# Kernel optimization log

Measured on AMD Instinct MI355X. Metric: run time of the kernel, lower is better.

Reference implementation:

```python
import jax, jax.numpy as jnp
import numpy as np

DIM = 2048
NH = 16
HD = DIM // NH          # 128
ROPE = 64               # qk_rope_head_dim
B = 2
S = 2048
LAYER_ID = 12
LAMBDA_INIT = float(0.8 - 0.6 * np.exp(-0.3 * LAYER_ID))
EPS = 1e-5


def _rope(x, cos, sin):
    # interleaved RoPE: pairs (x[2i], x[2i+1]) rotated by angle; x: [b,s,h,ROPE]
    xr = x[..., 0::2]
    xi = x[..., 1::2]
    c = cos[None, :, None, :]  # [1,s,1,ROPE/2]
    s_ = sin[None, :, None, :]
    yr = xr * c - xi * s_
    yi = xr * s_ + xi * c
    return jnp.stack([yr, yi], axis=-1).reshape(x.shape)


def _rope_head(t, cos, sin):
    # apply RoPE to first ROPE dims of head_dim, pass-through the rest
    return jnp.concatenate([_rope(t[..., :ROPE], cos, sin), t[..., ROPE:]], axis=-1)


def setup_inputs() -> dict:
    key = jax.random.key(0)
    ks = jax.random.split(key, 10)
    inner = 2 * NH * HD
    x = jax.random.normal(ks[0], (B, S, DIM), jnp.float32)
    w_q = jax.random.normal(ks[1], (inner, DIM), jnp.float32) * (DIM ** -0.5)
    w_k = jax.random.normal(ks[2], (inner, DIM), jnp.float32) * (DIM ** -0.5)
    w_v = jax.random.normal(ks[3], (inner, DIM), jnp.float32) * (DIM ** -0.5)
    w_o = jax.random.normal(ks[4], (DIM, inner), jnp.float32) * (inner ** -0.5)
    # lambda reparameterization params (paper uses small-std init for stability)
    lambda_q1 = jax.random.normal(ks[5], (NH, HD), jnp.float32) * 0.1
    lambda_k1 = jax.random.normal(ks[6], (NH, HD), jnp.float32) * 0.1
    lambda_q2 = jax.random.normal(ks[7], (NH, HD), jnp.float32) * 0.1
    lambda_k2 = jax.random.normal(ks[8], (NH, HD), jnp.float32) * 0.1
    rms_scale = jnp.ones((NH, 2 * HD), jnp.float32)
    # rotary frequencies
    pos = jnp.arange(S, dtype=jnp.float32)
    inv_freq = 1.0 / (10000.0 ** (jnp.arange(0, ROPE, 2, dtype=jnp.float32) / ROPE))
    ang = pos[:, None] * inv_freq[None, :]  # [S, ROPE/2]
    freqs_cos = jnp.cos(ang)
    freqs_sin = jnp.sin(ang)
    # additive causal mask
    mask = jnp.triu(jnp.full((S, S), -1e9, jnp.float32), k=1)
    return dict(x=x, w_q=w_q, w_k=w_k, w_v=w_v, w_o=w_o,
                lambda_q1=lambda_q1, lambda_k1=lambda_k1,
                lambda_q2=lambda_q2, lambda_k2=lambda_k2,
                rms_scale=rms_scale, freqs_cos=freqs_cos, freqs_sin=freqs_sin,
                mask=mask)


def reference(x, w_q, w_k, w_v, w_o, lambda_q1, lambda_k1, lambda_q2, lambda_k2,
              rms_scale, freqs_cos, freqs_sin, mask):
    b, s, _ = x.shape
    q = (x @ w_q.T).reshape(b, s, NH, 2 * HD)
    k = (x @ w_k.T).reshape(b, s, NH, 2 * HD)
    v = (x @ w_v.T).reshape(b, s, NH, 2 * HD)
    q1, q2 = jnp.split(q, 2, axis=-1)
    k1, k2 = jnp.split(k, 2, axis=-1)
    q1 = _rope_head(q1, freqs_cos, freqs_sin)
    q2 = _rope_head(q2, freqs_cos, freqs_sin)
    k1 = _rope_head(k1, freqs_cos, freqs_sin)
    k2 = _rope_head(k2, freqs_cos, freqs_sin)
    # start_pos = 0 prefill -> cache slice equals current k/v
    scale = HD ** -0.5
    s1 = jnp.einsum('bqhd,bkhd->bhqk', q1, k1) * scale + mask[None, None]
    s2 = jnp.einsum('bqhd,bkhd->bhqk', q2, k2) * scale + mask[None, None]
    a1 = jax.nn.softmax(s1, axis=-1)
    a2 = jax.nn.softmax(s2, axis=-1)
    lam1 = jnp.exp(jnp.sum(lambda_q1 * lambda_k1, axis=-1))  # [NH]
    lam2 = jnp.exp(jnp.sum(lambda_q2 * lambda_k2, axis=-1))
    lam = lam1 - lam2 + LAMBDA_INIT
    attn = a1 - lam[None, :, None, None] * a2
    o = jnp.einsum('bhqk,bkhd->bqhd', attn, v)  # [b,s,NH,2*HD]
    # headwise RMSNorm over 2*head_dim, then (1 - lambda_init) scaling
    o = o * jax.lax.rsqrt(jnp.mean(o * o, axis=-1, keepdims=True) + EPS)
    o = o * rms_scale[None, None] * (1.0 - LAMBDA_INIT)
    return o.reshape(b, s, 2 * NH * HD) @ w_o.T
```

## Files before the change

### kernel.cpp

```cpp
#include <hip/hip_runtime.h>

typedef __attribute__((ext_vector_type(8))) short s16x8;
typedef __attribute__((ext_vector_type(4))) short s16x4;
typedef __attribute__((ext_vector_type(4))) float f32x4;

#define NHh   16
#define Sd    2048
#define Bb    2
#define MSd   4096
#define DIMd  2048
#define INNERd 4096

constexpr float LAMBDA_INIT = 0.7836057665f;
constexpr float POST_SCALE  = 1.0f - LAMBDA_INIT;
constexpr float QK_SCALE    = 0.08838834764831845f;
constexpr float EPSf        = 1e-5f;

__device__ __forceinline__ short f2bf(float x) {
  unsigned u = __builtin_bit_cast(unsigned, x);
  u = (u + 0x7fffu + ((u >> 16) & 1u)) >> 16;
  return (short)u;
}
__device__ __forceinline__ float bf2f(short x) {
  unsigned u = ((unsigned)(unsigned short)x) << 16;
  return __builtin_bit_cast(float, u);
}
__device__ __forceinline__ f32x4 mfma16(s16x8 a, s16x8 b, f32x4 c) {
  return __builtin_amdgcn_mfma_f32_16x16x32_bf16(a, b, c, 0, 0, 0);
}
__device__ __forceinline__ void async16(void* lds, const void* g) {
  __builtin_amdgcn_global_load_lds(
      (const __attribute__((address_space(1))) void*)g,
      (__attribute__((address_space(3))) void*)lds, 16, 0, 0);
}

__global__ __launch_bounds__(256)
void convert5(const float* __restrict__ a0, const float* __restrict__ a1,
              const float* __restrict__ a2, const float* __restrict__ a3,
              const float* __restrict__ a4,
              short* __restrict__ o0, short* __restrict__ o1,
              short* __restrict__ o2, short* __restrict__ o3,
              short* __restrict__ o4) {
  const float* src; short* dst;
  switch (blockIdx.y) {
    case 0: src = a0; dst = o0; break;
    case 1: src = a1; dst = o1; break;
    case 2: src = a2; dst = o2; break;
    case 3: src = a3; dst = o3; break;
    default: src = a4; dst = o4; break;
  }
  size_t i = ((size_t)blockIdx.x * 256 + threadIdx.x) * 4;
  f32x4 x = *(const f32x4*)(src + i);
  s16x4 o;
#pragma unroll
  for (int j = 0; j < 4; ++j) o[j] = f2bf(x[j]);
  *(s16x4*)(dst + i) = o;
}

__global__ void lambda_kernel(const float* __restrict__ lq1, const float* __restrict__ lk1,
                              const float* __restrict__ lq2, const float* __restrict__ lk2,
                              float* __restrict__ lam) {
  int h = threadIdx.x;
  if (h < NHh) {
    float s1 = 0.f, s2 = 0.f;
    for (int d = 0; d < 128; ++d) {
      s1 += lq1[h * 128 + d] * lk1[h * 128 + d];
      s2 += lq2[h * 128 + d] * lk2[h * 128 + d];
    }
    lam[h] = expf(s1) - expf(s2) + LAMBDA_INIT;
  }
}

template <typename OutT>
__global__ __launch_bounds__(256)
void gemm_bt(const short* __restrict__ A, const short* __restrict__ Bm,
             OutT* __restrict__ C, int M, int N, int K) {
  __shared__ __align__(16) short As[128 * 32];
  __shared__ __align__(16) short Bs[128 * 32];
  const int tid  = threadIdx.x;
  const int lane = tid & 63;
  const int w    = tid >> 6;
  const int wr   = (w >> 1) * 64;
  const int wc   = (w & 1) * 64;
  const int m0   = blockIdx.x * 128;
  const int n0   = blockIdx.y * 128;
  const int l15  = lane & 15, l4 = lane >> 4;

  f32x4 acc[4][4] = {};

  for (int kt = 0; kt < K; kt += 32) {
#pragma unroll
    for (int j = 0; j < 2; ++j) {
      int L  = j * 4096 + tid * 16;
      int r  = L >> 6;
      int s  = (L >> 4) & 3;
      int sp = s ^ ((r >> 1) & 3);
      async16((char*)As + L, A  + (size_t)(m0 + r) * K + kt + sp * 8);
      async16((char*)Bs + L, Bm + (size_t)(n0 + r) * K + kt + sp * 8);
    }
    __syncthreads();

    s16x8 af[4], bf[4];
#pragma unroll
    for (int mi = 0; mi < 4; ++mi) {
      int r  = wr + mi * 16 + l15;
      int sl = l4 ^ ((r >> 1) & 3);
      af[mi] = *(const s16x8*)(As + r * 32 + sl * 8);
    }
#pragma unroll
    for (int ni = 0; ni < 4; ++ni) {
      int r  = wc + ni * 16 + l15;
      int sl = l4 ^ ((r >> 1) & 3);
      bf[ni] = *(const s16x8*)(Bs + r * 32 + sl * 8);
    }
#pragma unroll
    for (int mi = 0; mi < 4; ++mi)
#pragma unroll
      for (int ni = 0; ni < 4; ++ni)
        acc[mi][ni] = mfma16(af[mi], bf[ni], acc[mi][ni]);
    __syncthreads();
  }

#pragma unroll
  for (int mi = 0; mi < 4; ++mi)
#pragma unroll
    for (int ni = 0; ni < 4; ++ni)
#pragma unroll
      for (int j = 0; j < 4; ++j) {
        int row = m0 + wr + mi * 16 + l4 * 4 + j;
        int col = n0 + wc + ni * 16 + l15;
        float v = acc[mi][ni][j];
        if constexpr (sizeof(OutT) == 2) C[(size_t)row * N + col] = f2bf(v);
        else                             C[(size_t)row * N + col] = v;
      }
}

__global__ __launch_bounds__(256)
void rope_qk(short* __restrict__ qp, short* __restrict__ kp,
             const float* __restrict__ fc, const float* __restrict__ fs) {
  int idx  = blockIdx.x * 256 + threadIdx.x;
  int ib   = idx & 7;
  int half = (idx >> 3) & 1;
  int h    = (idx >> 4) & 15;
  int s    = (idx >> 8) & 2047;
  int b    = (idx >> 19) & 1;
  short* base = (idx >> 20) ? kp : qp;
  size_t off  = ((size_t)(b * Sd + s) * NHh + h) * 256 + half * 128 + ib * 8;
  s16x8 v = *(s16x8*)(base + off);
  f32x4 c  = *(const f32x4*)(fc + s * 32 + ib * 4);
  f32x4 sn = *(const f32x4*)(fs + s * 32 + ib * 4);
#pragma unroll
  for (int p = 0; p < 4; ++p) {
    float xr = bf2f(v[2 * p]), xi = bf2f(v[2 * p + 1]);
    float yr = xr * c[p] - xi * sn[p];
    float yi = xr * sn[p] + xi * c[p];
    v[2 * p]     = f2bf(yr);
    v[2 * p + 1] = f2bf(yi);
  }
  *(s16x8*)(base + off) = v;
}

__global__ __launch_bounds__(256)
void transpose_v(const short* __restrict__ v, short* __restrict__ vt) {
  __shared__ __align__(16) short t[64][80];
  const int s0 = blockIdx.x * 64;
  const int d0 = blockIdx.y * 64;
  const int bh = blockIdx.z;
  const int b  = bh >> 4, h = bh & 15;
  const int tid = threadIdx.x;
#pragma unroll
  for (int rp = 0; rp < 2; ++rp) {
    int i  = rp * 256 + tid;
    int sl = i >> 3;
    int dl = (i & 7) * 8;
    s16x8 x = *(const s16x8*)(v + ((size_t)(b * Sd + s0 + sl) * NHh + h) * 256 + d0 + dl);
    *(s16x8*)(&t[sl][dl]) = x;
  }
  __syncthreads();
#pragma unroll
  for (int rp = 0; rp < 2; ++rp) {
    int i   = rp * 256 + tid;
    int dl  = i >> 3;
    int sp8 = (i & 7) * 8;
    s16x8 x;
#pragma unroll
    for (int j = 0; j < 8; ++j) x[j] = t[sp8 + j][dl];
    *(s16x8*)(vt + ((size_t)bh * 256 + d0 + dl) * Sd + s0 + sp8) = x;
  }
}

__global__ __launch_bounds__(256)
void flash_diff(const short* __restrict__ q, const short* __restrict__ k,
                const short* __restrict__ vt, const float* __restrict__ lam,
                const float* __restrict__ rms_scale, short* __restrict__ obuf) {
  const int qt = blockIdx.x, h = blockIdx.y, b = blockIdx.z;
  const int tid = threadIdx.x;
  const int lane = tid & 63, w = tid >> 6;
  const int q0 = qt * 64;
  const int wrow0 = q0 + w * 16;
  const int l15 = lane & 15, l4 = lane >> 4;

  __shared__ __align__(16) short K1s[32 * 128];
  __shared__ __align__(16) short K2s[32 * 128];
  __shared__ __align__(16) short Vs[256 * 32];
  __shared__ __align__(16) short Ps[4][2][512];

  s16x8 q1f[4], q2f[4];
  {
    const size_t qrow = ((size_t)(b * Sd + wrow0 + l15) * NHh + h) * 256;
#pragma unroll
    for (int kb = 0; kb < 4; ++kb) {
      q1f[kb] = *(const s16x8*)(q + qrow + kb * 32 + l4 * 8);
      q2f[kb] = *(const s16x8*)(q + qrow + 128 + kb * 32 + l4 * 8);
    }
  }

  float m1[4], l1[4], m2[4], l2[4];
#pragma unroll
  for (int j = 0; j < 4; ++j) { m1[j] = m2[j] = -1e30f; l1[j] = l2[j] = 0.f; }
  f32x4 O1[16] = {};
  f32x4 O2[16] = {};

  const int kv_end = q0 + 64;
  for (int kv0 = 0; kv0 < kv_end; kv0 += 32) {
#pragma unroll
    for (int j = 0; j < 2; ++j) {
      int L  = j * 4096 + tid * 16;
      int r  = L >> 8;
      int s  = (L >> 4) & 15;
      int sp = s ^ (r & 7);
      const size_t krow = ((size_t)(b * Sd + kv0 + r) * NHh + h) * 256;
      async16((char*)K1s + L, k + krow + sp * 8);
      async16((char*)K2s + L, k + krow + 128 + sp * 8);
    }
#pragma unroll
    for (int j = 0; j < 4; ++j) {
      int L  = j * 4096 + tid * 16;
      int r  = L >> 6;
      int s  = (L >> 4) & 3;
      int sp = s ^ ((r >> 1) & 3);
      async16((char*)Vs + L, vt + ((size_t)(b * NHh + h) * 256 + r) * Sd + kv0 + sp * 8);
    }
    __syncthreads();

    if (kv0 <= wrow0 + 15) {
      f32x4 s1[2] = {}, s2[2] = {};
#pragma unroll
      for (int kb = 0; kb < 4; ++kb)
#pragma unroll
        for (int cf = 0; cf < 2; ++cf) {
          int r  = cf * 16 + l15;
          int sl = (kb * 4 + l4) ^ (r & 7);
          s16x8 kf1 = *(const s16x8*)(K1s + r * 128 + sl * 8);
          s16x8 kf2 = *(const s16x8*)(K2s + r * 128 + sl * 8);
          s1[cf] = mfma16(q1f[kb], kf1, s1[cf]);
          s2[cf] = mfma16(q2f[kb], kf2, s2[cf]);
        }

      float sv1[2][4], sv2[2][4];
#pragma unroll
      for (int cf = 0; cf < 2; ++cf)
#pragma unroll
        for (int j = 0; j < 4; ++j) {
          int kvc = kv0 + cf * 16 + l15;
          int row = wrow0 + l4 * 4 + j;
          bool msk = kvc > row;
          sv1[cf][j] = msk ? -1e9f : s1[cf][j] * QK_SCALE;
          sv2[cf][j] = msk ? -1e9f : s2[cf][j] * QK_SCALE;
        }

      auto online = [&](float (&sv)[2][4], float (&m)[4], float (&l)[4],
                        f32x4 (&O)[16], short* pbuf) {
        float tmax[4], rs[4], ps[4];
#pragma unroll
        for (int j = 0; j < 4; ++j) tmax[j] = fmaxf(sv[0][j], sv[1][j]);
#pragma unroll
        for (int j = 0; j < 4; ++j) {
          tmax[j] = fmaxf(tmax[j], __shfl_xor(tmax[j], 1));
          tmax[j] = fmaxf(tmax[j], __shfl_xor(tmax[j], 2));
          tmax[j] = fmaxf(tmax[j], __shfl_xor(tmax[j], 4));
          tmax[j] = fmaxf(tmax[j], __shfl_xor(tmax[j], 8));
        }
#pragma unroll
        for (int j = 0; j < 4; ++j) {
          float mn = fmaxf(m[j], tmax[j]);
          rs[j] = __expf(m[j] - mn);
          m[j] = mn;
          ps[j] = 0.f;
        }
#pragma unroll
        for (int cf = 0; cf < 2; ++cf)
#pragma unroll
          for (int j = 0; j < 4; ++j) {
            float p = __expf(sv[cf][j] - m[j]);
            ps[j] += p;
            pbuf[(l4 * 4 + j) * 32 + cf * 16 + l15] = f2bf(p);
          }
#pragma unroll
        for (int j = 0; j < 4; ++j) {
          ps[j] += __shfl_xor(ps[j], 1);
          ps[j] += __shfl_xor(ps[j], 2);
          ps[j] += __shfl_xor(ps[j], 4);
          ps[j] += __shfl_xor(ps[j], 8);
          l[j] = l[j] * rs[j] + ps[j];
        }
#pragma unroll
        for (int nf = 0; nf < 16; ++nf) {
          O[nf][0] *= rs[0]; O[nf][1] *= rs[1];
          O[nf][2] *= rs[2]; O[nf][3] *= rs[3];
        }
      };
      online(sv1, m1, l1, O1, &Ps[w][0][0]);
      online(sv2, m2, l2, O2, &Ps[w][1][0]);

      s16x8 pa1 = *(const s16x8*)(&Ps[w][0][0] + l15 * 32 + l4 * 8);
      s16x8 pa2 = *(const s16x8*)(&Ps[w][1][0] + l15 * 32 + l4 * 8);
#pragma unroll
      for (int nf = 0; nf < 16; ++nf) {
        int d  = nf * 16 + l15;
        int sl = l4 ^ ((d >> 1) & 3);
        s16x8 vf = *(const s16x8*)(Vs + d * 32 + sl * 8);
        O1[nf] = mfma16(pa1, vf, O1[nf]);
        O2[nf] = mfma16(pa2, vf, O2[nf]);
      }
    }
    __syncthreads();
  }

  const float lamh = lam[h];
  float inv1[4], inv2[4], ss[4];
#pragma unroll
  for (int j = 0; j < 4; ++j) {
    inv1[j] = 1.f / l1[j];
    inv2[j] = 1.f / l2[j];
    ss[j] = 0.f;
  }
#pragma unroll
  for (int nf = 0; nf < 16; ++nf)
#pragma unroll
    for (int j = 0; j < 4; ++j) {
      float o = O1[nf][j] * inv1[j] - lamh * O2[nf][j] * inv2[j];
      O1[nf][j] = o;
      ss[j] += o * o;
    }
#pragma unroll
  for (int j = 0; j < 4; ++j) {
    ss[j] += __shfl_xor(ss[j], 1);
    ss[j] += __shfl_xor(ss[j], 2);
    ss[j] += __shfl_xor(ss[j], 4);
    ss[j] += __shfl_xor(ss[j], 8);
    ss[j] = rsqrtf(ss[j] * (1.f / 256.f) + EPSf);
  }
#pragma unroll
  for (int nf = 0; nf < 16; ++nf) {
    float sc = rms_scale[h * 256 + nf * 16 + l15] * POST_SCALE;
#pragma unroll
    for (int j = 0; j < 4; ++j) {
      float v = O1[nf][j] * ss[j] * sc;
      obuf[((size_t)(b * Sd + wrow0 + l4 * 4 + j) * NHh + h) * 256 + nf * 16 + l15] = f2bf(v);
    }
  }
}

extern "C" void kernel_launch(void* const* d_in, const int* in_sizes, int n_in,
                              void* d_out, int out_size, void* d_ws, size_t ws_size,
                              hipStream_t stream) {
  const float* x   = (const float*)d_in[0];
  const float* w_q = (const float*)d_in[1];
  const float* w_k = (const float*)d_in[2];
  const float* w_v = (const float*)d_in[3];
  const float* w_o = (const float*)d_in[4];
  const float* lq1 = (const float*)d_in[5];
  const float* lk1 = (const float*)d_in[6];
  const float* lq2 = (const float*)d_in[7];
  const float* lk2 = (const float*)d_in[8];
  const float* rms = (const float*)d_in[9];
  const float* fc  = (const float*)d_in[10];
  const float* fs  = (const float*)d_in[11];

  char* ws = (char*)d_ws;
  const size_t SMb = 16777216ull;
  const size_t BGb = 33554432ull;
  short* xb  = (short*)(ws);
  short* wqb = (short*)(ws + 1 * SMb);
  short* wkb = (short*)(ws + 2 * SMb);
  short* wvb = (short*)(ws + 3 * SMb);
  short* wob = (short*)(ws + 4 * SMb);
  short* qb  = (short*)(ws + 5 * SMb);
  short* kb  = (short*)(ws + 5 * SMb + 1 * BGb);
  short* vb  = (short*)(ws + 5 * SMb + 2 * BGb);
  short* vtb = (short*)(ws + 5 * SMb + 3 * BGb);
  short* ob  = (short*)(ws + 5 * SMb + 4 * BGb);
  float* lam = (float*)(ws + 5 * SMb + 5 * BGb);

  convert5<<<dim3(8192, 5), 256, 0, stream>>>(x, w_q, w_k, w_v, w_o,
                                              xb, wqb, wkb, wvb, wob);
  lambda_kernel<<<1, 64, 0, stream>>>(lq1, lk1, lq2, lk2, lam);
  gemm_bt<short><<<dim3(32, 32), 256, 0, stream>>>(xb, wqb, qb, 4096, 4096, 2048);
  gemm_bt<short><<<dim3(32, 32), 256, 0, stream>>>(xb, wkb, kb, 4096, 4096, 2048);
  gemm_bt<short><<<dim3(32, 32), 256, 0, stream>>>(xb, wvb, vb, 4096, 4096, 2048);
  rope_qk<<<8192, 256, 0, stream>>>(qb, kb, fc, fs);
  transpose_v<<<dim3(32, 4, 32), 256, 0, stream>>>(vb, vtb);
  flash_diff<<<dim3(32, 16, 2), 256, 0, stream>>>(qb, kb, vtb, lam, rms, ob);
  gemm_bt<float><<<dim3(32, 16), 256, 0, stream>>>(ob, wob, (float*)d_out, 4096, 2048, 4096);
}
```

Measured before the change: 1.373 ms.

## Double-buffer KV tiles, reverse query-tile order, swizzle GEMM blocks, pad P buffer

The flash attention kernel now double-buffers the K1/K2/V shared-memory tiles, issuing the async load for the next tile before computing on the current one, and drops one barrier per iteration. Query tiles are launched in reverse order so the heaviest causal blocks are scheduled first. The P scratch buffer row stride is padded from 32 to 40 shorts to reduce LDS bank conflicts. The GEMM remaps block IDs in an XCD-style round-robin of 8 to improve L2 locality. Doubling the shared memory use may lower occupancy.

```diff
diff --git a/kernel.cpp b/kernel.cpp
--- a/kernel.cpp
+++ b/kernel.cpp
@@ -82,8 +82,14 @@
   const int w    = tid >> 6;
   const int wr   = (w >> 1) * 64;
   const int wc   = (w & 1) * 64;
-  const int m0   = blockIdx.x * 128;
-  const int n0   = blockIdx.y * 128;
+
+  const int nb  = gridDim.x * gridDim.y;
+  const int id  = blockIdx.y * gridDim.x + blockIdx.x;
+  const int cpx = nb >> 3;
+  const int sw  = (id & 7) * cpx + (id >> 3);
+  const int m0  = (sw % gridDim.x) * 128;
+  const int n0  = (sw / gridDim.x) * 128;
+
   const int l15  = lane & 15, l4 = lane >> 4;
 
   f32x4 acc[4][4] = {};
@@ -193,36 +199,20 @@
 void flash_diff(const short* __restrict__ q, const short* __restrict__ k,
                 const short* __restrict__ vt, const float* __restrict__ lam,
                 const float* __restrict__ rms_scale, short* __restrict__ obuf) {
-  const int qt = blockIdx.x, h = blockIdx.y, b = blockIdx.z;
+  const int qt = gridDim.x - 1 - blockIdx.x;
+  const int h = blockIdx.y, b = blockIdx.z;
   const int tid = threadIdx.x;
   const int lane = tid & 63, w = tid >> 6;
   const int q0 = qt * 64;
   const int wrow0 = q0 + w * 16;
   const int l15 = lane & 15, l4 = lane >> 4;
 
-  __shared__ __align__(16) short K1s[32 * 128];
-  __shared__ __align__(16) short K2s[32 * 128];
-  __shared__ __align__(16) short Vs[256 * 32];
-  __shared__ __align__(16) short Ps[4][2][512];
-
-  s16x8 q1f[4], q2f[4];
-  {
-    const size_t qrow = ((size_t)(b * Sd + wrow0 + l15) * NHh + h) * 256;
-#pragma unroll
-    for (int kb = 0; kb < 4; ++kb) {
-      q1f[kb] = *(const s16x8*)(q + qrow + kb * 32 + l4 * 8);
-      q2f[kb] = *(const s16x8*)(q + qrow + 128 + kb * 32 + l4 * 8);
-    }
-  }
-
-  float m1[4], l1[4], m2[4], l2[4];
-#pragma unroll
-  for (int j = 0; j < 4; ++j) { m1[j] = m2[j] = -1e30f; l1[j] = l2[j] = 0.f; }
-  f32x4 O1[16] = {};
-  f32x4 O2[16] = {};
-
-  const int kv_end = q0 + 64;
-  for (int kv0 = 0; kv0 < kv_end; kv0 += 32) {
+  __shared__ __align__(16) short K1s[2][32 * 128];
+  __shared__ __align__(16) short K2s[2][32 * 128];
+  __shared__ __align__(16) short Vs[2][256 * 32];
+  __shared__ __align__(16) short Ps[4][2][16 * 40];
+
+  auto stage = [&](int bf, int kv0) {
 #pragma unroll
     for (int j = 0; j < 2; ++j) {
       int L  = j * 4096 + tid * 16;
@@ -230,8 +220,8 @@
       int s  = (L >> 4) & 15;
       int sp = s ^ (r & 7);
       const size_t krow = ((size_t)(b * Sd + kv0 + r) * NHh + h) * 256;
-      async16((char*)K1s + L, k + krow + sp * 8);
-      async16((char*)K2s + L, k + krow + 128 + sp * 8);
+      async16((char*)&K1s[bf][0] + L, k + krow + sp * 8);
+      async16((char*)&K2s[bf][0] + L, k + krow + 128 + sp * 8);
     }
 #pragma unroll
     for (int j = 0; j < 4; ++j) {
@@ -239,9 +229,34 @@
       int r  = L >> 6;
       int s  = (L >> 4) & 3;
       int sp = s ^ ((r >> 1) & 3);
-      async16((char*)Vs + L, vt + ((size_t)(b * NHh + h) * 256 + r) * Sd + kv0 + sp * 8);
-    }
+      async16((char*)&Vs[bf][0] + L, vt + ((size_t)(b * NHh + h) * 256 + r) * Sd + kv0 + sp * 8);
+    }
+  };
+
+  s16x8 q1f[4], q2f[4];
+  {
+    const size_t qrow = ((size_t)(b * Sd + wrow0 + l15) * NHh + h) * 256;
+#pragma unroll
+    for (int kb = 0; kb < 4; ++kb) {
+      q1f[kb] = *(const s16x8*)(q + qrow + kb * 32 + l4 * 8);
+      q2f[kb] = *(const s16x8*)(q + qrow + 128 + kb * 32 + l4 * 8);
+    }
+  }
+
+  float m1[4], l1[4], m2[4], l2[4];
+#pragma unroll
+  for (int j = 0; j < 4; ++j) { m1[j] = m2[j] = -1e30f; l1[j] = l2[j] = 0.f; }
+  f32x4 O1[16] = {};
+  f32x4 O2[16] = {};
+
+  const int nst = qt * 2 + 2;
+  stage(0, 0);
+
+  for (int t = 0; t < nst; ++t) {
     __syncthreads();
+    if (t + 1 < nst) stage((t + 1) & 1, (t + 1) * 32);
+    const int kv0 = t * 32;
+    const int cur = t & 1;
 
     if (kv0 <= wrow0 + 15) {
       f32x4 s1[2] = {}, s2[2] = {};
@@ -251,8 +266,8 @@
         for (int cf = 0; cf < 2; ++cf) {
           int r  = cf * 16 + l15;
           int sl = (kb * 4 + l4) ^ (r & 7);
-          s16x8 kf1 = *(const s16x8*)(K1s + r * 128 + sl * 8);
-          s16x8 kf2 = *(const s16x8*)(K2s + r * 128 + sl * 8);
+          s16x8 kf1 = *(const s16x8*)(&K1s[cur][0] + r * 128 + sl * 8);
+          s16x8 kf2 = *(const s16x8*)(&K2s[cur][0] + r * 128 + sl * 8);
           s1[cf] = mfma16(q1f[kb], kf1, s1[cf]);
           s2[cf] = mfma16(q2f[kb], kf2, s2[cf]);
         }
@@ -294,7 +309,7 @@
           for (int j = 0; j < 4; ++j) {
             float p = __expf(sv[cf][j] - m[j]);
             ps[j] += p;
-            pbuf[(l4 * 4 + j) * 32 + cf * 16 + l15] = f2bf(p);
+            pbuf[(l4 * 4 + j) * 40 + cf * 16 + l15] = f2bf(p);
           }
 #pragma unroll
         for (int j = 0; j < 4; ++j) {
@@ -313,18 +328,17 @@
       online(sv1, m1, l1, O1, &Ps[w][0][0]);
       online(sv2, m2, l2, O2, &Ps[w][1][0]);
 
-      s16x8 pa1 = *(const s16x8*)(&Ps[w][0][0] + l15 * 32 + l4 * 8);
-      s16x8 pa2 = *(const s16x8*)(&Ps[w][1][0] + l15 * 32 + l4 * 8);
+      s16x8 pa1 = *(const s16x8*)(&Ps[w][0][0] + l15 * 40 + l4 * 8);
+      s16x8 pa2 = *(const s16x8*)(&Ps[w][1][0] + l15 * 40 + l4 * 8);
 #pragma unroll
       for (int nf = 0; nf < 16; ++nf) {
         int d  = nf * 16 + l15;
         int sl = l4 ^ ((d >> 1) & 3);
-        s16x8 vf = *(const s16x8*)(Vs + d * 32 + sl * 8);
+        s16x8 vf = *(const s16x8*)(&Vs[cur][0] + d * 32 + sl * 8);
         O1[nf] = mfma16(pa1, vf, O1[nf]);
         O2[nf] = mfma16(pa2, vf, O2[nf]);
       }
     }
-    __syncthreads();
   }
 
   const float lamh = lam[h];
```

Result: slower. 1.455 ms (+6.0%).
